# Optimization experiments

Hardware: AMD Instinct MI355X
Metric: run time of the kernel (lower is better)

The kernel has to match this reference:

```python
import jax, jax.numpy as jnp
import numpy as np

HIDDEN = 2048
N_HEADS = 16
N_KV = 4
HEAD_DIM = 128
SEQ = 2048
BATCH = 2
THETA = 10000.0


def rotate_half(x):
    half = x.shape[-1] // 2
    x1, x2 = x[..., :half], x[..., half:]
    return jnp.concatenate((-x2, x1), axis=-1)


def rope_cos_sin(seq_len, dim, theta, dtype):
    inv_freq = 1.0 / (theta ** (jnp.arange(0, dim, 2, dtype=jnp.float32) / dim))
    t = jnp.arange(seq_len, dtype=jnp.float32)
    freqs = jnp.einsum('i,j->ij', t, inv_freq)            # [S, dim/2]
    emb = jnp.concatenate((freqs, freqs), axis=-1)        # [S, dim]
    return jnp.cos(emb).astype(dtype), jnp.sin(emb).astype(dtype)


def setup_inputs() -> dict:
    key = jax.random.key(0)
    kx, kq, kk, kv, ko = jax.random.split(key, 5)
    s = 0.02
    return {
        'x':  jax.random.normal(kx, (BATCH, SEQ, HIDDEN), dtype=jnp.float32),
        'Wq': jax.random.normal(kq, (HIDDEN, N_HEADS * HEAD_DIM), dtype=jnp.float32) * s,
        'Wk': jax.random.normal(kk, (HIDDEN, N_KV * HEAD_DIM), dtype=jnp.float32) * s,
        'Wv': jax.random.normal(kv, (HIDDEN, N_KV * HEAD_DIM), dtype=jnp.float32) * s,
        'Wo': jax.random.normal(ko, (N_HEADS * HEAD_DIM, HIDDEN), dtype=jnp.float32) * s,
    }


def reference(x, Wq, Wk, Wv, Wo):
    B, S, _ = x.shape
    q = (x @ Wq).reshape(B, S, N_HEADS, HEAD_DIM)
    k = (x @ Wk).reshape(B, S, N_KV, HEAD_DIM)
    v = (x @ Wv).reshape(B, S, N_KV, HEAD_DIM)

    cos, sin = rope_cos_sin(S, HEAD_DIM, THETA, x.dtype)
    cos = cos[None, :, None, :]  # [1,S,1,D]
    sin = sin[None, :, None, :]
    q = q * cos + rotate_half(q) * sin
    k = k * cos + rotate_half(k) * sin

    repeat = N_HEADS // N_KV
    k = jnp.repeat(k, repeat, axis=2)  # repeat_interleave over heads
    v = jnp.repeat(v, repeat, axis=2)

    # [B,H,S,D]
    q = q.transpose(0, 2, 1, 3)
    k = k.transpose(0, 2, 1, 3)
    v = v.transpose(0, 2, 1, 3)

    scale = HEAD_DIM ** -0.5
    scores = jnp.einsum('bhqd,bhkd->bhqk', q, k) * scale
    causal = jnp.triu(jnp.full((S, S), -jnp.inf, dtype=scores.dtype), k=1)
    scores = scores + causal
    probs = jax.nn.softmax(scores, axis=-1)
    out = jnp.einsum('bhqk,bhkd->bhqd', probs, v)
    out = out.transpose(0, 2, 1, 3).reshape(B, S, N_HEADS * HEAD_DIM)
    return out @ Wo
```

## Files before the change

### kernel.cpp

```cpp
#include <hip/hip_runtime.h>
#include <hip/hip_bf16.h>
#include <math.h>

#define HIDDEN 2048
#define NHEADS 16
#define NKV 4
#define HD 128
#define SEQ 2048
#define BATCH 2
#define MTOT (BATCH*SEQ)
#define NQ (NHEADS*HD)
#define NKVD (NKV*HD)
#define NQKV (NQ + 2*NKVD)

typedef __attribute__((ext_vector_type(8))) short short8;
typedef __attribute__((ext_vector_type(4))) float float4v;

#if __has_builtin(__builtin_amdgcn_exp2f)
#define EXP2F __builtin_amdgcn_exp2f
#else
#define EXP2F exp2f
#endif
#define C1 0.1275174f

static __device__ __forceinline__ unsigned short f2bf(float f) {
  union { float f; unsigned int u; } v; v.f = f;
  unsigned int r = v.u + 0x7FFF + ((v.u >> 16) & 1);
  return (unsigned short)(r >> 16);
}
static __device__ __forceinline__ float bf2f(unsigned short h) {
  union { unsigned int u; float f; } v; v.u = ((unsigned int)h) << 16;
  return v.f;
}

static __device__ __forceinline__ void async16(const unsigned short* g, unsigned short* l) {
  __builtin_amdgcn_global_load_lds(
      (const __attribute__((address_space(1))) unsigned int*)g,
      (__attribute__((address_space(3))) unsigned int*)l, 16, 0, 0);
}

__global__ void cast_f32_bf16(const float* __restrict__ in,
                              unsigned short* __restrict__ out, int n) {
  int i = (blockIdx.x * blockDim.x + threadIdx.x) * 4;
  if (i < n) {
    float4 v = *(const float4*)(in + i);
    ushort4 o;
    o.x = f2bf(v.x); o.y = f2bf(v.y); o.z = f2bf(v.z); o.w = f2bf(v.w);
    *(ushort4*)(out + i) = o;
  }
}

__global__ void transpose_cast_all(
    const float* __restrict__ Wq, const float* __restrict__ Wk,
    const float* __restrict__ Wv, const float* __restrict__ Wo,
    unsigned short* __restrict__ Wqt, unsigned short* __restrict__ Wkt,
    unsigned short* __restrict__ Wvt, unsigned short* __restrict__ Wot) {
  __shared__ float tile[32][33];
  const int K = 2048;
  int bx = blockIdx.x;
  const float* W; unsigned short* Wt; int N; int tn;
  if (bx < 64)      { W = Wq; Wt = Wqt; N = NQ;     tn = bx * 32; }
  else if (bx < 80) { W = Wk; Wt = Wkt; N = NKVD;   tn = (bx - 64) * 32; }
  else if (bx < 96) { W = Wv; Wt = Wvt; N = NKVD;   tn = (bx - 80) * 32; }
  else              { W = Wo; Wt = Wot; N = HIDDEN; tn = (bx - 96) * 32; }
  int tk = blockIdx.y * 32;
  int tx = threadIdx.x & 31;
  int ty = threadIdx.x >> 5;
  #pragma unroll
  for (int i = 0; i < 4; i++) {
    int k = tk + ty + i * 8;
    tile[ty + i * 8][tx] = W[(size_t)k * N + tn + tx];
  }
  __syncthreads();
  #pragma unroll
  for (int i = 0; i < 4; i++) {
    int n = tn + ty + i * 8;
    Wt[(size_t)n * K + tk + tx] = f2bf(tile[tx][ty + i * 8]);
  }
}

__global__ void rope_all(unsigned short* __restrict__ Qb,
                         unsigned short* __restrict__ Kb) {
  int idx = blockIdx.x * blockDim.x + threadIdx.x;
  const int QTOT = MTOT * NHEADS * 64;
  unsigned short* P; int nheads;
  if (idx < QTOT) { P = Qb; nheads = NHEADS; }
  else            { P = Kb; nheads = NKV; idx -= QTOT; }
  int d = idx & 63;
  int hr = idx >> 6;
  int spos = (hr / nheads) % SEQ;
  size_t base = (size_t)hr * HD;
  float inv = exp2f((float)d * -0.2076205059304601f);
  float ang = (float)spos * inv;
  float sn, cs;
  sincosf(ang, &sn, &cs);
  float q1 = bf2f(P[base + d]);
  float q2 = bf2f(P[base + d + 64]);
  P[base + d]      = f2bf(q1 * cs - q2 * sn);
  P[base + d + 64] = f2bf(q2 * cs + q1 * sn);
}

__global__ __launch_bounds__(512, 2) void gemm_qkv(
    const unsigned short* __restrict__ A,
    const unsigned short* __restrict__ Bt,
    unsigned short* __restrict__ Qb,
    unsigned short* __restrict__ Kb,
    unsigned short* __restrict__ Vt) {
  __shared__ __align__(16) unsigned short L[4 * 16384];
  const int K = HIDDEN;
  const int NT = K / 32;
  int bm = blockIdx.y * 256, bn = blockIdx.x * 256;
  int tid = threadIdx.x, w = tid >> 6, lane = tid & 63;
  int wrow = w >> 2, wcol = w & 3;
  int m16 = lane & 15, quad = lane >> 4;
  int lrow = lane >> 2, lch = lane & 3;
  int lchs = lch ^ ((lrow >> 1) & 3);
  int qx = quad ^ ((m16 >> 1) & 3);
  const unsigned short* Ag = A + (size_t)(bm + w * 32 + lrow) * K + lchs * 8;
  const unsigned short* Bg = Bt + (size_t)(bn + w * 32 + lrow) * K + lchs * 8;

  float4v acc[8][4];
  #pragma unroll
  for (int i = 0; i < 8; i++)
    #pragma unroll
    for (int j = 0; j < 4; j++) acc[i][j] = (float4v)0.0f;

  auto stage = [&](int t) {
    unsigned short* Lb = L + (t & 3) * 16384;
    int k0 = t * 32;
    #pragma unroll
    for (int i = 0; i < 2; i++) {
      async16(Ag + (size_t)i * 16 * K + k0, Lb + w * 1024 + i * 512);
      async16(Bg + (size_t)i * 16 * K + k0, Lb + 8192 + w * 1024 + i * 512);
    }
  };

  const bool isV = (blockIdx.x >= 10);

  stage(0); stage(1);
  asm volatile("s_waitcnt vmcnt(4)" ::: "memory");
  __builtin_amdgcn_s_barrier();
  __builtin_amdgcn_sched_barrier(0);

  if (!isV) {
    for (int t = 0; t < NT; ++t) {
      if (t + 2 < NT) stage(t + 2);
      const unsigned short* Ab_ = L + (t & 3) * 16384;
      const unsigned short* Bb_ = Ab_ + 8192;
      short8 af[8], bfr[4];
      #pragma unroll
      for (int i = 0; i < 8; i++)
        af[i] = *(const short8*)(&Ab_[(wrow * 128 + i * 16 + m16) * 32 + qx * 8]);
      #pragma unroll
      for (int j = 0; j < 4; j++)
        bfr[j] = *(const short8*)(&Bb_[(wcol * 64 + j * 16 + m16) * 32 + qx * 8]);
      __builtin_amdgcn_s_setprio(1);
      #pragma unroll
      for (int i = 0; i < 8; i++)
        #pragma unroll
        for (int j = 0; j < 4; j++)
          acc[i][j] = __builtin_amdgcn_mfma_f32_16x16x32_bf16(af[i], bfr[j], acc[i][j], 0, 0, 0);
      __builtin_amdgcn_s_setprio(0);
      if (t + 2 < NT) { asm volatile("s_waitcnt vmcnt(4)" ::: "memory"); }
      else            { asm volatile("s_waitcnt vmcnt(0)" ::: "memory"); }
      __builtin_amdgcn_s_barrier();
      __builtin_amdgcn_sched_barrier(0);
    }
  } else {
    for (int t = 0; t < NT; ++t) {
      if (t + 2 < NT) stage(t + 2);
      const unsigned short* Ab_ = L + (t & 3) * 16384;
      const unsigned short* Bb_ = Ab_ + 8192;
      short8 af[8], bfr[4];
      #pragma unroll
      for (int i = 0; i < 8; i++)
        af[i] = *(const short8*)(&Ab_[(wrow * 128 + i * 16 + m16) * 32 + qx * 8]);
      #pragma unroll
      for (int j = 0; j < 4; j++)
        bfr[j] = *(const short8*)(&Bb_[(wcol * 64 + j * 16 + m16) * 32 + qx * 8]);
      __builtin_amdgcn_s_setprio(1);
      #pragma unroll
      for (int i = 0; i < 8; i++)
        #pragma unroll
        for (int j = 0; j < 4; j++)
          acc[i][j] = __builtin_amdgcn_mfma_f32_16x16x32_bf16(bfr[j], af[i], acc[i][j], 0, 0, 0);
      __builtin_amdgcn_s_setprio(0);
      if (t + 2 < NT) { asm volatile("s_waitcnt vmcnt(4)" ::: "memory"); }
      else            { asm volatile("s_waitcnt vmcnt(0)" ::: "memory"); }
      __builtin_amdgcn_s_barrier();
      __builtin_amdgcn_sched_barrier(0);
    }
  }

  if (blockIdx.x < 8) {
    #pragma unroll
    for (int i = 0; i < 8; i++)
      #pragma unroll
      for (int j = 0; j < 4; j++)
        #pragma unroll
        for (int r = 0; r < 4; r++) {
          int row = bm + wrow * 128 + i * 16 + quad * 4 + r;
          int col = bn + wcol * 64 + j * 16 + m16;
          Qb[(size_t)row * NQ + col] = f2bf(acc[i][j][r]);
        }
  } else if (!isV) {
    #pragma unroll
    for (int i = 0; i < 8; i++)
      #pragma unroll
      for (int j = 0; j < 4; j++)
        #pragma unroll
        for (int r = 0; r < 4; r++) {
          int row = bm + wrow * 128 + i * 16 + quad * 4 + r;
          int col = bn - 2048 + wcol * 64 + j * 16 + m16;
          Kb[(size_t)row * NKVD + col] = f2bf(acc[i][j][r]);
        }
  } else {
    #pragma unroll
    for (int i = 0; i < 8; i++)
      #pragma unroll
      for (int j = 0; j < 4; j++)
        #pragma unroll
        for (int r = 0; r < 4; r++) {
          int f = bn - 2560 + wcol * 64 + j * 16 + quad * 4 + r;
          int m = bm + wrow * 128 + i * 16 + m16;
          Vt[(size_t)f * MTOT + m] = f2bf(acc[i][j][r]);
        }
  }
}

__global__ __launch_bounds__(256, 2) void gemm_o(
    const unsigned short* __restrict__ A,
    const unsigned short* __restrict__ Bt,
    float* __restrict__ C, int M, int N, int K) {
  __shared__ __align__(16) unsigned short L[4 * 8192];
  const int NT = K / 32;
  int bm = blockIdx.y * 128, bn = blockIdx.x * 128;
  int tid = threadIdx.x, w = tid >> 6, lane = tid & 63;
  int wm = (w >> 1) * 64, wn = (w & 1) * 64;
  int m16 = lane & 15, quad = lane >> 4;
  int lrow = lane >> 2, lch = lane & 3;
  int lchs = lch ^ ((lrow >> 1) & 3);
  int qx = quad ^ ((m16 >> 1) & 3);
  const unsigned short* Ag = A + (size_t)(bm + w * 32 + lrow) * K + lchs * 8;
  const unsigned short* Bg = Bt + (size_t)(bn + w * 32 + lrow) * K + lchs * 8;

  float4v acc[4][4];
  #pragma unroll
  for (int i = 0; i < 4; i++)
    #pragma unroll
    for (int j = 0; j < 4; j++) acc[i][j] = (float4v)0.0f;

  auto stage = [&](int t) {
    unsigned short* Lb = L + (t & 3) * 8192;
    int k0 = t * 32;
    #pragma unroll
    for (int i = 0; i < 2; i++) {
      async16(Ag + (size_t)i * 16 * K + k0, Lb + w * 1024 + i * 512);
      async16(Bg + (size_t)i * 16 * K + k0, Lb + 4096 + w * 1024 + i * 512);
    }
  };

  stage(0); stage(1);
  asm volatile("s_waitcnt vmcnt(4)" ::: "memory");
  __builtin_amdgcn_s_barrier();
  __builtin_amdgcn_sched_barrier(0);

  for (int t = 0; t < NT; ++t) {
    if (t + 2 < NT) stage(t + 2);
    const unsigned short* Ab_ = L + (t & 3) * 8192;
    const unsigned short* Bb_ = Ab_ + 4096;
    short8 af[4], bfr[4];
    #pragma unroll
    for (int i = 0; i < 4; i++)
      af[i] = *(const short8*)(&Ab_[(wm + i * 16 + m16) * 32 + qx * 8]);
    #pragma unroll
    for (int j = 0; j < 4; j++)
      bfr[j] = *(const short8*)(&Bb_[(wn + j * 16 + m16) * 32 + qx * 8]);
    __builtin_amdgcn_s_setprio(1);
    #pragma unroll
    for (int i = 0; i < 4; i++)
      #pragma unroll
      for (int j = 0; j < 4; j++)
        acc[i][j] = __builtin_amdgcn_mfma_f32_16x16x32_bf16(af[i], bfr[j], acc[i][j], 0, 0, 0);
    __builtin_amdgcn_s_setprio(0);
    if (t + 2 < NT) { asm volatile("s_waitcnt vmcnt(4)" ::: "memory"); }
    else            { asm volatile("s_waitcnt vmcnt(0)" ::: "memory"); }
    __builtin_amdgcn_s_barrier();
    __builtin_amdgcn_sched_barrier(0);
  }

  #pragma unroll
  for (int i = 0; i < 4; i++)
    #pragma unroll
    for (int j = 0; j < 4; j++)
      #pragma unroll
      for (int r = 0; r < 4; r++) {
        int row = bm + wm + i * 16 + quad * 4 + r;
        int col = bn + wn + j * 16 + m16;
        C[(size_t)row * N + col] = acc[i][j][r];
      }
}

#define FLASH_TILE(CUR, NXT)                                                  \
  {                                                                           \
    const int ktb = kt * 64;                                                  \
    __syncthreads();        \
    {                                                                         \
      const unsigned short* Vg = Vt + vgrow * (size_t)MTOT                    \
                                    + (size_t)b * SEQ + ktb + kcv * 32 + vlch * 8; \
      unsigned short* Vl = Vs + kcv * 4096 + ipv * 512;                       \
      _Pragma("unroll")                                                       \
      for (int i = 0; i < 4; i++) async16(Vg + (size_t)i * 16 * MTOT, Vl + i * 512); \
    }                                                                         \
    if (kt < H) {                                                             \
      const unsigned short* Kg = Kp + (((size_t)b * SEQ + (kt + 1) * 64 + lrow) * NKV + kvh) * HD + w * 32 + vlch * 8; \
      unsigned short* Kl = NXT + w * 2048;                                    \
      _Pragma("unroll")                                                       \
      for (int i = 0; i < 4; i++) async16(Kg + (size_t)i * 16 * NKV * HD, Kl + i * 512); \
    }                                                                         \
    const bool act1 = (ktb <= lmax_w);                                        \
    float4v sacc[2][4];                                                       \
    _Pragma("unroll") for (int s4 = 0; s4 < 4; s4++) {                        \
      sacc[0][s4] = (float4v)0.0f; sacc[1][s4] = (float4v)0.0f; }             \
    __builtin_amdgcn_s_setprio(1);                                            \
    if (act1) {                                                               \
      _Pragma("unroll")                                                       \
      for (int s4 = 0; s4 < 4; s4++)                                          \
        _Pragma("unroll")                                                     \
        for (int c = 0; c < 4; c++) {                                         \
          short8 kf = *(const short8*)(&CUR[c * 2048 + (s4 * 16 + m16) * 32 + qx * 8]); \
          sacc[0][s4] = __builtin_amdgcn_mfma_f32_16x16x32_bf16(kf, qf[0][c], sacc[0][s4], 0, 0, 0); \
          sacc[1][s4] = __builtin_amdgcn_mfma_f32_16x16x32_bf16(kf, qf[1][c], sacc[1][s4], 0, 0, 0); \
        }                                                                     \
    } else {                                                                  \
      _Pragma("unroll")                                                       \
      for (int s4 = 0; s4 < 4; s4++)                                          \
        _Pragma("unroll")                                                     \
        for (int c = 0; c < 4; c++) {                                         \
          short8 kf = *(const short8*)(&CUR[c * 2048 + (s4 * 16 + m16) * 32 + qx * 8]); \
          sacc[0][s4] = __builtin_amdgcn_mfma_f32_16x16x32_bf16(kf, qf[0][c], sacc[0][s4], 0, 0, 0); \
        }                                                                     \
    }                                                                         \
    __builtin_amdgcn_s_setprio(0);                                            \
    _Pragma("unroll")                                                         \
    for (int qs = 0; qs < 2; qs++) {                                          \
      if (qs == 0 || act1) {                                                  \
        const int tb = qs ? L : H;                                            \
        const int qabs = tb * 64 + w * 16 + m16;                              \
        const bool diag = (kt == tb);                                         \
        float sv[4][4]; float mloc = -1e30f;                                  \
        if (diag) {                                                           \
          _Pragma("unroll") for (int s4 = 0; s4 < 4; s4++)                    \
            _Pragma("unroll") for (int r = 0; r < 4; r++) {                   \
              int kabs = ktb + s4 * 16 + quad * 4 + r;                        \
              float t = sacc[qs][s4][r];                                      \
              sv[s4][r] = (kabs > qabs) ? -1e30f : t;                         \
              mloc = fmaxf(mloc, sv[s4][r]); }                                \
        } else {                                                              \
          _Pragma("unroll") for (int s4 = 0; s4 < 4; s4++)                    \
            _Pragma("unroll") for (int r = 0; r < 4; r++) {                   \
              sv[s4][r] = sacc[qs][s4][r]; mloc = fmaxf(mloc, sv[s4][r]); }   \
        }                                                                     \
        mloc *= C1;                                                           \
        mloc = fmaxf(mloc, __shfl_xor(mloc, 16, 64));                         \
        mloc = fmaxf(mloc, __shfl_xor(mloc, 32, 64));                         \
        float mnewS = fmaxf(miS[qs], mloc);                                   \
        const bool defer = (bool)__all(mloc <= miS[qs] + 8.0f);               \
        if (defer) mnewS = miS[qs];  \
        const int prow = qs * 64 + w * 16 + m16;                              \
        const int psw = prow * 32; const int rx = prow & 7;                   \
        float rs = 0.0f;                                                      \
        _Pragma("unroll") for (int s4 = 0; s4 < 4; s4++) {                    \
          float p0 = EXP2F(__builtin_fmaf(sv[s4][0], C1, -mnewS));            \
          float p1 = EXP2F(__builtin_fmaf(sv[s4][1], C1, -mnewS));            \
          float p2 = EXP2F(__builtin_fmaf(sv[s4][2], C1, -mnewS));            \
          float p3 = EXP2F(__builtin_fmaf(sv[s4][3], C1, -mnewS));            \
          rs += p0 + p1 + p2 + p3;                                            \
          uint2 u;                                                            \
          u.x = (__float_as_uint(p1) & 0xffff0000u) | (__float_as_uint(p0) >> 16); \
          u.y = (__float_as_uint(p3) & 0xffff0000u) | (__float_as_uint(p2) >> 16); \
          int chunkW = s4 * 2 + (quad >> 1);                                  \
          *(uint2*)(&Ps[psw + ((chunkW ^ rx) << 2) + (quad & 1) * 2]) = u;    \
        }                                                                     \
        rs += __shfl_xor(rs, 16, 64);                                         \
        rs += __shfl_xor(rs, 32, 64);                                         \
        if (!defer) {                                                         \
          const float alpha = EXP2F(miS[qs] - mnewS);                         \
          li[qs] *= alpha; miS[qs] = mnewS;                                   \
          _Pragma("unroll") for (int ds = 0; ds < 8; ds++) oacc[ds][qs] *= alpha; \
        }                                                                     \
        li[qs] += rs;                                                         \
      }                                                                       \
    }                                                                         \
    __syncthreads();     \
    {                                                                         \
      const int r0 = w * 16 + m16, r1 = 64 + w * 16 + m16;                    \
      __builtin_amdgcn_s_setprio(1);                                          \
      if (act1) {                                                             \
        _Pragma("unroll")                                                     \
        for (int kc = 0; kc < 2; kc++) {                                      \
          short8 pf0 = *(const short8*)(&Ps[r0 * 32 + (((kc * 4 + quad) ^ (r0 & 7)) << 2)]); \
          short8 pf1 = *(const short8*)(&Ps[r1 * 32 + (((kc * 4 + quad) ^ (r1 & 7)) << 2)]); \
          _Pragma("unroll")                                                   \
          for (int ds = 0; ds < 8; ds++) {                                    \
            short8 vf = *(const short8*)(&Vs[kc * 4096 + (ds * 16 + m16) * 32 + qx * 8]); \
            oacc[ds][0] = __builtin_amdgcn_mfma_f32_16x16x32_bf16(vf, pf0, oacc[ds][0], 0, 0, 0); \
            oacc[ds][1] = __builtin_amdgcn_mfma_f32_16x16x32_bf16(vf, pf1, oacc[ds][1], 0, 0, 0); \
          }                                                                   \
        }                                                                     \
      } else {                                                                \
        _Pragma("unroll")                                                     \
        for (int kc = 0; kc < 2; kc++) {                                      \
          short8 pf0 = *(const short8*)(&Ps[r0 * 32 + (((kc * 4 + quad) ^ (r0 & 7)) << 2)]); \
          _Pragma("unroll")                                                   \
          for (int ds = 0; ds < 8; ds++) {                                    \
            short8 vf = *(const short8*)(&Vs[kc * 4096 + (ds * 16 + m16) * 32 + qx * 8]); \
            oacc[ds][0] = __builtin_amdgcn_mfma_f32_16x16x32_bf16(vf, pf0, oacc[ds][0], 0, 0, 0); \
          }                                                                   \
        }                                                                     \
      }                                                                       \
      __builtin_amdgcn_s_setprio(0);                                          \
    }                                                                         \
  }

__global__ __launch_bounds__(256, 2) void flash_attn(
    const unsigned short* __restrict__ Q,
    const unsigned short* __restrict__ Kp,
    const unsigned short* __restrict__ Vt,
    unsigned short* __restrict__ O) {
  __shared__ unsigned short Ks0[4 * 64 * 32];
  __shared__ unsigned short Ks1[4 * 64 * 32];
  __shared__ unsigned short Vs[2 * 128 * 32];
  __shared__ unsigned int   Ps[128 * 32];

  int bx = blockIdx.x;
  int h  = blockIdx.y;
  int b  = blockIdx.z;
  int kvh = h >> 2;
  int H = 31 - bx, L = bx;
  int tid = threadIdx.x;
  int w = tid >> 6, lane = tid & 63;
  int m16 = lane & 15, quad = lane >> 4;
  int lrow = lane >> 2, lch = lane & 3;
  const int vlch = lch ^ ((lrow >> 1) & 3);
  const int qx = quad ^ ((m16 >> 1) & 3);
  const int lmax_w = L * 64 + w * 16 + 15;

  const int kcv = w >> 1, ipv = (w & 1) * 4;
  const size_t vgrow = (size_t)kvh * HD + ipv * 16 + lrow;

  short8 qf[2][4];
  #pragma unroll
  for (int qs = 0; qs < 2; qs++) {
    int tb = qs ? L : H;
    size_t qbase = (((size_t)b * SEQ + tb * 64 + w * 16 + m16) * NHEADS + h) * HD;
    #pragma unroll
    for (int c = 0; c < 4; c++)
      qf[qs][c] = *(const short8*)(Q + qbase + c * 32 + quad * 8);
  }

  float4v oacc[8][2];
  #pragma unroll
  for (int ds = 0; ds < 8; ds++) { oacc[ds][0] = (float4v)0.0f; oacc[ds][1] = (float4v)0.0f; }
  float miS[2] = {-1e30f, -1e30f}, li[2] = {0.0f, 0.0f};

  {
    const unsigned short* Kg = Kp + (((size_t)b * SEQ + lrow) * NKV + kvh) * HD + w * 32 + vlch * 8;
    unsigned short* Kl = Ks0 + w * 2048;
    #pragma unroll
    for (int i = 0; i < 4; i++) async16(Kg + (size_t)i * 16 * NKV * HD, Kl + i * 512);
  }

  int kt = 0;
  for (;;) {
    FLASH_TILE(Ks0, Ks1)
    if (++kt > H) break;
    FLASH_TILE(Ks1, Ks0)
    if (++kt > H) break;
  }

  #pragma unroll
  for (int qs = 0; qs < 2; qs++) {
    float inv = 1.0f / li[qs];
    int tb = qs ? L : H;
    int qabs = tb * 64 + w * 16 + m16;
    size_t obase = (((size_t)b * SEQ + qabs) * NHEADS + h) * HD + quad * 4;
    #pragma unroll
    for (int ds = 0; ds < 8; ds++) {
      float v0 = oacc[ds][qs][0] * inv;
      float v1 = oacc[ds][qs][1] * inv;
      float v2 = oacc[ds][qs][2] * inv;
      float v3 = oacc[ds][qs][3] * inv;
      uint2 u;
      u.x = ((unsigned)f2bf(v1) << 16) | f2bf(v0);
      u.y = ((unsigned)f2bf(v3) << 16) | f2bf(v2);
      *(uint2*)(O + obase + ds * 16) = u;
    }
  }
}

extern "C" void kernel_launch(void* const* d_in, const int* in_sizes, int n_in,
                              void* d_out, int out_size, void* d_ws, size_t ws_size,
                              hipStream_t stream) {
  const float* x  = (const float*)d_in[0];
  const float* Wq = (const float*)d_in[1];
  const float* Wk = (const float*)d_in[2];
  const float* Wv = (const float*)d_in[3];
  const float* Wo = (const float*)d_in[4];
  float* out = (float*)d_out;

  unsigned short* ws = (unsigned short*)d_ws;
  unsigned short* xb  = ws;
  unsigned short* Wqt = xb  + (size_t)MTOT * HIDDEN;
  unsigned short* Wkt = Wqt + (size_t)NQ * HIDDEN;
  unsigned short* Wvt = Wkt + (size_t)NKVD * HIDDEN;
  unsigned short* Wot = Wvt + (size_t)NKVD * HIDDEN;
  unsigned short* Qb  = Wot + (size_t)NQ * HIDDEN;
  unsigned short* Kb  = Qb  + (size_t)MTOT * NQ;
  unsigned short* Vtb = Kb  + (size_t)MTOT * NKVD;
  unsigned short* Ab  = Vtb + (size_t)MTOT * NKVD;

  cast_f32_bf16<<<(MTOT * HIDDEN / 4 + 255) / 256, 256, 0, stream>>>(x, xb, MTOT * HIDDEN);
  transpose_cast_all<<<dim3(160, 64), 256, 0, stream>>>(Wq, Wk, Wv, Wo, Wqt, Wkt, Wvt, Wot);

  gemm_qkv<<<dim3(NQKV / 256, MTOT / 256), 512, 0, stream>>>(xb, Wqt, Qb, Kb, Vtb);

  rope_all<<<(MTOT * (NHEADS + NKV) * 64) / 256, 256, 0, stream>>>(Qb, Kb);

  flash_attn<<<dim3(16, NHEADS, BATCH), 256, 0, stream>>>(Qb, Kb, Vtb, Ab);

  gemm_o<<<dim3(HIDDEN / 128, MTOT / 128), 256, 0, stream>>>(Ab, Wot, out, MTOT, HIDDEN, NQ);
}
```

Measured before the change: 286.3 us.

## Merge prep kernels, fuse Q RoPE into attention, double GEMM wave counts

Merges the x cast and weight transpose-cast into one prep launch. Q RoPE is now applied in registers inside flash attention, so rope only runs on K, which removes a full read and write pass over Q. Both GEMMs double threads per block (1024 and 512) and give each wave a smaller sub-tile, with one async load per thread per stage. This trades fewer launches and less Q traffic for per-wave sincos work in attention and different GEMM occupancy and register behaviour.

```diff
diff --git a/kernel.cpp b/kernel.cpp
--- a/kernel.cpp
+++ b/kernel.cpp
@@ -39,31 +39,30 @@
       (__attribute__((address_space(3))) unsigned int*)l, 16, 0, 0);
 }
 
-__global__ void cast_f32_bf16(const float* __restrict__ in,
-                              unsigned short* __restrict__ out, int n) {
-  int i = (blockIdx.x * blockDim.x + threadIdx.x) * 4;
-  if (i < n) {
-    float4 v = *(const float4*)(in + i);
+__global__ void prep(const float* __restrict__ x, unsigned short* __restrict__ xb,
+                     const float* __restrict__ Wq, const float* __restrict__ Wk,
+                     const float* __restrict__ Wv, const float* __restrict__ Wo,
+                     unsigned short* __restrict__ Wqt, unsigned short* __restrict__ Wkt,
+                     unsigned short* __restrict__ Wvt, unsigned short* __restrict__ Wot) {
+  __shared__ float tile[32][33];
+  int bx = blockIdx.x;
+  if (bx < 8192) {
+    int i = (bx * 256 + threadIdx.x) * 4;
+    float4 v = *(const float4*)(x + i);
     ushort4 o;
     o.x = f2bf(v.x); o.y = f2bf(v.y); o.z = f2bf(v.z); o.w = f2bf(v.w);
-    *(ushort4*)(out + i) = o;
-  }
-}
-
-__global__ void transpose_cast_all(
-    const float* __restrict__ Wq, const float* __restrict__ Wk,
-    const float* __restrict__ Wv, const float* __restrict__ Wo,
-    unsigned short* __restrict__ Wqt, unsigned short* __restrict__ Wkt,
-    unsigned short* __restrict__ Wvt, unsigned short* __restrict__ Wot) {
-  __shared__ float tile[32][33];
+    *(ushort4*)(xb + i) = o;
+    return;
+  }
+  int bz = bx - 8192;
+  int tbx = bz % 160, tby = bz / 160;
   const int K = 2048;
-  int bx = blockIdx.x;
   const float* W; unsigned short* Wt; int N; int tn;
-  if (bx < 64)      { W = Wq; Wt = Wqt; N = NQ;     tn = bx * 32; }
-  else if (bx < 80) { W = Wk; Wt = Wkt; N = NKVD;   tn = (bx - 64) * 32; }
-  else if (bx < 96) { W = Wv; Wt = Wvt; N = NKVD;   tn = (bx - 80) * 32; }
-  else              { W = Wo; Wt = Wot; N = HIDDEN; tn = (bx - 96) * 32; }
-  int tk = blockIdx.y * 32;
+  if (tbx < 64)      { W = Wq; Wt = Wqt; N = NQ;     tn = tbx * 32; }
+  else if (tbx < 80) { W = Wk; Wt = Wkt; N = NKVD;   tn = (tbx - 64) * 32; }
+  else if (tbx < 96) { W = Wv; Wt = Wvt; N = NKVD;   tn = (tbx - 80) * 32; }
+  else               { W = Wo; Wt = Wot; N = HIDDEN; tn = (tbx - 96) * 32; }
+  int tk = tby * 32;
   int tx = threadIdx.x & 31;
   int ty = threadIdx.x >> 5;
   #pragma unroll
@@ -79,28 +78,23 @@
   }
 }
 
-__global__ void rope_all(unsigned short* __restrict__ Qb,
-                         unsigned short* __restrict__ Kb) {
+__global__ void rope_k(unsigned short* __restrict__ Kb) {
   int idx = blockIdx.x * blockDim.x + threadIdx.x;
-  const int QTOT = MTOT * NHEADS * 64;
-  unsigned short* P; int nheads;
-  if (idx < QTOT) { P = Qb; nheads = NHEADS; }
-  else            { P = Kb; nheads = NKV; idx -= QTOT; }
   int d = idx & 63;
   int hr = idx >> 6;
-  int spos = (hr / nheads) % SEQ;
+  int spos = (hr / NKV) % SEQ;
   size_t base = (size_t)hr * HD;
   float inv = exp2f((float)d * -0.2076205059304601f);
   float ang = (float)spos * inv;
   float sn, cs;
   sincosf(ang, &sn, &cs);
-  float q1 = bf2f(P[base + d]);
-  float q2 = bf2f(P[base + d + 64]);
-  P[base + d]      = f2bf(q1 * cs - q2 * sn);
-  P[base + d + 64] = f2bf(q2 * cs + q1 * sn);
-}
-
-__global__ __launch_bounds__(512, 2) void gemm_qkv(
+  float q1 = bf2f(Kb[base + d]);
+  float q2 = bf2f(Kb[base + d + 64]);
+  Kb[base + d]      = f2bf(q1 * cs - q2 * sn);
+  Kb[base + d + 64] = f2bf(q2 * cs + q1 * sn);
+}
+
+__global__ __launch_bounds__(1024, 4) void gemm_qkv(
     const unsigned short* __restrict__ A,
     const unsigned short* __restrict__ Bt,
     unsigned short* __restrict__ Qb,
@@ -113,32 +107,29 @@
   int tid = threadIdx.x, w = tid >> 6, lane = tid & 63;
   int wrow = w >> 2, wcol = w & 3;
   int m16 = lane & 15, quad = lane >> 4;
-  int lrow = lane >> 2, lch = lane & 3;
-  int lchs = lch ^ ((lrow >> 1) & 3);
+  int r = tid >> 2, lch = tid & 3;
+  int lchs = lch ^ ((r >> 1) & 3);
   int qx = quad ^ ((m16 >> 1) & 3);
-  const unsigned short* Ag = A + (size_t)(bm + w * 32 + lrow) * K + lchs * 8;
-  const unsigned short* Bg = Bt + (size_t)(bn + w * 32 + lrow) * K + lchs * 8;
-
-  float4v acc[8][4];
-  #pragma unroll
-  for (int i = 0; i < 8; i++)
+  const unsigned short* Agp = A + (size_t)(bm + r) * K + lchs * 8;
+  const unsigned short* Bgp = Bt + (size_t)(bn + r) * K + lchs * 8;
+
+  float4v acc[4][4];
+  #pragma unroll
+  for (int i = 0; i < 4; i++)
     #pragma unroll
     for (int j = 0; j < 4; j++) acc[i][j] = (float4v)0.0f;
 
   auto stage = [&](int t) {
     unsigned short* Lb = L + (t & 3) * 16384;
     int k0 = t * 32;
-    #pragma unroll
-    for (int i = 0; i < 2; i++) {
-      async16(Ag + (size_t)i * 16 * K + k0, Lb + w * 1024 + i * 512);
-      async16(Bg + (size_t)i * 16 * K + k0, Lb + 8192 + w * 1024 + i * 512);
-    }
+    async16(Agp + k0, Lb + tid * 8);
+    async16(Bgp + k0, Lb + 8192 + tid * 8);
   };
 
   const bool isV = (blockIdx.x >= 10);
 
   stage(0); stage(1);
-  asm volatile("s_waitcnt vmcnt(4)" ::: "memory");
+  asm volatile("s_waitcnt vmcnt(2)" ::: "memory");
   __builtin_amdgcn_s_barrier();
   __builtin_amdgcn_sched_barrier(0);
 
@@ -147,21 +138,21 @@
       if (t + 2 < NT) stage(t + 2);
       const unsigned short* Ab_ = L + (t & 3) * 16384;
       const unsigned short* Bb_ = Ab_ + 8192;
-      short8 af[8], bfr[4];
-      #pragma unroll
-      for (int i = 0; i < 8; i++)
-        af[i] = *(const short8*)(&Ab_[(wrow * 128 + i * 16 + m16) * 32 + qx * 8]);
+      short8 af[4], bfr[4];
+      #pragma unroll
+      for (int i = 0; i < 4; i++)
+        af[i] = *(const short8*)(&Ab_[(wrow * 64 + i * 16 + m16) * 32 + qx * 8]);
       #pragma unroll
       for (int j = 0; j < 4; j++)
         bfr[j] = *(const short8*)(&Bb_[(wcol * 64 + j * 16 + m16) * 32 + qx * 8]);
       __builtin_amdgcn_s_setprio(1);
       #pragma unroll
-      for (int i = 0; i < 8; i++)
+      for (int i = 0; i < 4; i++)
         #pragma unroll
         for (int j = 0; j < 4; j++)
           acc[i][j] = __builtin_amdgcn_mfma_f32_16x16x32_bf16(af[i], bfr[j], acc[i][j], 0, 0, 0);
       __builtin_amdgcn_s_setprio(0);
-      if (t + 2 < NT) { asm volatile("s_waitcnt vmcnt(4)" ::: "memory"); }
+      if (t + 2 < NT) { asm volatile("s_waitcnt vmcnt(2)" ::: "memory"); }
       else            { asm volatile("s_waitcnt vmcnt(0)" ::: "memory"); }
       __builtin_amdgcn_s_barrier();
       __builtin_amdgcn_sched_barrier(0);
@@ -171,21 +162,21 @@
       if (t + 2 < NT) stage(t + 2);
       const unsigned short* Ab_ = L + (t & 3) * 16384;
       const unsigned short* Bb_ = Ab_ + 8192;
-      short8 af[8], bfr[4];
-      #pragma unroll
-      for (int i = 0; i < 8; i++)
-        af[i] = *(const short8*)(&Ab_[(wrow * 128 + i * 16 + m16) * 32 + qx * 8]);
+      short8 af[4], bfr[4];
+      #pragma unroll
+      for (int i = 0; i < 4; i++)
+        af[i] = *(const short8*)(&Ab_[(wrow * 64 + i * 16 + m16) * 32 + qx * 8]);
       #pragma unroll
       for (int j = 0; j < 4; j++)
         bfr[j] = *(const short8*)(&Bb_[(wcol * 64 + j * 16 + m16) * 32 + qx * 8]);
       __builtin_amdgcn_s_setprio(1);
       #pragma unroll
-      for (int i = 0; i < 8; i++)
+      for (int i = 0; i < 4; i++)
         #pragma unroll
         for (int j = 0; j < 4; j++)
           acc[i][j] = __builtin_amdgcn_mfma_f32_16x16x32_bf16(bfr[j], af[i], acc[i][j], 0, 0, 0);
       __builtin_amdgcn_s_setprio(0);
-      if (t + 2 < NT) { asm volatile("s_waitcnt vmcnt(4)" ::: "memory"); }
+      if (t + 2 < NT) { asm volatile("s_waitcnt vmcnt(2)" ::: "memory"); }
       else            { asm volatile("s_waitcnt vmcnt(0)" ::: "memory"); }
       __builtin_amdgcn_s_barrier();
       __builtin_amdgcn_sched_barrier(0);
@@ -194,41 +185,41 @@
 
   if (blockIdx.x < 8) {
     #pragma unroll
-    for (int i = 0; i < 8; i++)
+    for (int i = 0; i < 4; i++)
       #pragma unroll
       for (int j = 0; j < 4; j++)
         #pragma unroll
-        for (int r = 0; r < 4; r++) {
-          int row = bm + wrow * 128 + i * 16 + quad * 4 + r;
+        for (int rr = 0; rr < 4; rr++) {
+          int row = bm + wrow * 64 + i * 16 + quad * 4 + rr;
           int col = bn + wcol * 64 + j * 16 + m16;
-          Qb[(size_t)row * NQ + col] = f2bf(acc[i][j][r]);
+          Qb[(size_t)row * NQ + col] = f2bf(acc[i][j][rr]);
         }
   } else if (!isV) {
     #pragma unroll
-    for (int i = 0; i < 8; i++)
+    for (int i = 0; i < 4; i++)
       #pragma unroll
       for (int j = 0; j < 4; j++)
         #pragma unroll
-        for (int r = 0; r < 4; r++) {
-          int row = bm + wrow * 128 + i * 16 + quad * 4 + r;
+        for (int rr = 0; rr < 4; rr++) {
+          int row = bm + wrow * 64 + i * 16 + quad * 4 + rr;
           int col = bn - 2048 + wcol * 64 + j * 16 + m16;
-          Kb[(size_t)row * NKVD + col] = f2bf(acc[i][j][r]);
+          Kb[(size_t)row * NKVD + col] = f2bf(acc[i][j][rr]);
         }
   } else {
     #pragma unroll
-    for (int i = 0; i < 8; i++)
+    for (int i = 0; i < 4; i++)
       #pragma unroll
       for (int j = 0; j < 4; j++)
         #pragma unroll
-        for (int r = 0; r < 4; r++) {
-          int f = bn - 2560 + wcol * 64 + j * 16 + quad * 4 + r;
-          int m = bm + wrow * 128 + i * 16 + m16;
-          Vt[(size_t)f * MTOT + m] = f2bf(acc[i][j][r]);
+        for (int rr = 0; rr < 4; rr++) {
+          int f = bn - 2560 + wcol * 64 + j * 16 + quad * 4 + rr;
+          int m = bm + wrow * 64 + i * 16 + m16;
+          Vt[(size_t)f * MTOT + m] = f2bf(acc[i][j][rr]);
         }
   }
 }
 
-__global__ __launch_bounds__(256, 2) void gemm_o(
+__global__ __launch_bounds__(512, 4) void gemm_o(
     const unsigned short* __restrict__ A,
     const unsigned short* __restrict__ Bt,
     float* __restrict__ C, int M, int N, int K) {
@@ -236,32 +227,29 @@
   const int NT = K / 32;
   int bm = blockIdx.y * 128, bn = blockIdx.x * 128;
   int tid = threadIdx.x, w = tid >> 6, lane = tid & 63;
-  int wm = (w >> 1) * 64, wn = (w & 1) * 64;
+  int wrow = w >> 2, wcol = w & 3;
   int m16 = lane & 15, quad = lane >> 4;
-  int lrow = lane >> 2, lch = lane & 3;
-  int lchs = lch ^ ((lrow >> 1) & 3);
+  int r = tid >> 2, lch = tid & 3;
+  int lchs = lch ^ ((r >> 1) & 3);
   int qx = quad ^ ((m16 >> 1) & 3);
-  const unsigned short* Ag = A + (size_t)(bm + w * 32 + lrow) * K + lchs * 8;
-  const unsigned short* Bg = Bt + (size_t)(bn + w * 32 + lrow) * K + lchs * 8;
-
-  float4v acc[4][4];
+  const unsigned short* Agp = A + (size_t)(bm + r) * K + lchs * 8;
+  const unsigned short* Bgp = Bt + (size_t)(bn + r) * K + lchs * 8;
+
+  float4v acc[4][2];
   #pragma unroll
   for (int i = 0; i < 4; i++)
     #pragma unroll
-    for (int j = 0; j < 4; j++) acc[i][j] = (float4v)0.0f;
+    for (int j = 0; j < 2; j++) acc[i][j] = (float4v)0.0f;
 
   auto stage = [&](int t) {
     unsigned short* Lb = L + (t & 3) * 8192;
     int k0 = t * 32;
-    #pragma unroll
-    for (int i = 0; i < 2; i++) {
-      async16(Ag + (size_t)i * 16 * K + k0, Lb + w * 1024 + i * 512);
-      async16(Bg + (size_t)i * 16 * K + k0, Lb + 4096 + w * 1024 + i * 512);
-    }
+    async16(Agp + k0, Lb + tid * 8);
+    async16(Bgp + k0, Lb + 4096 + tid * 8);
   };
 
   stage(0); stage(1);
-  asm volatile("s_waitcnt vmcnt(4)" ::: "memory");
+  asm volatile("s_waitcnt vmcnt(2)" ::: "memory");
   __builtin_amdgcn_s_barrier();
   __builtin_amdgcn_sched_barrier(0);
 
@@ -269,21 +257,21 @@
     if (t + 2 < NT) stage(t + 2);
     const unsigned short* Ab_ = L + (t & 3) * 8192;
     const unsigned short* Bb_ = Ab_ + 4096;
-    short8 af[4], bfr[4];
+    short8 af[4], bfr[2];
     #pragma unroll
     for (int i = 0; i < 4; i++)
-      af[i] = *(const short8*)(&Ab_[(wm + i * 16 + m16) * 32 + qx * 8]);
-    #pragma unroll
-    for (int j = 0; j < 4; j++)
-      bfr[j] = *(const short8*)(&Bb_[(wn + j * 16 + m16) * 32 + qx * 8]);
+      af[i] = *(const short8*)(&Ab_[(wrow * 64 + i * 16 + m16) * 32 + qx * 8]);
+    #pragma unroll
+    for (int j = 0; j < 2; j++)
+      bfr[j] = *(const short8*)(&Bb_[(wcol * 32 + j * 16 + m16) * 32 + qx * 8]);
     __builtin_amdgcn_s_setprio(1);
     #pragma unroll
     for (int i = 0; i < 4; i++)
       #pragma unroll
-      for (int j = 0; j < 4; j++)
+      for (int j = 0; j < 2; j++)
         acc[i][j] = __builtin_amdgcn_mfma_f32_16x16x32_bf16(af[i], bfr[j], acc[i][j], 0, 0, 0);
     __builtin_amdgcn_s_setprio(0);
-    if (t + 2 < NT) { asm volatile("s_waitcnt vmcnt(4)" ::: "memory"); }
+    if (t + 2 < NT) { asm volatile("s_waitcnt vmcnt(2)" ::: "memory"); }
     else            { asm volatile("s_waitcnt vmcnt(0)" ::: "memory"); }
     __builtin_amdgcn_s_barrier();
     __builtin_amdgcn_sched_barrier(0);
@@ -292,12 +280,12 @@
   #pragma unroll
   for (int i = 0; i < 4; i++)
     #pragma unroll
-    for (int j = 0; j < 4; j++)
-      #pragma unroll
-      for (int r = 0; r < 4; r++) {
-        int row = bm + wm + i * 16 + quad * 4 + r;
-        int col = bn + wn + j * 16 + m16;
-        C[(size_t)row * N + col] = acc[i][j][r];
+    for (int j = 0; j < 2; j++)
+      #pragma unroll
+      for (int rr = 0; rr < 4; rr++) {
+        int row = bm + wrow * 64 + i * 16 + quad * 4 + rr;
+        int col = bn + wcol * 32 + j * 16 + m16;
+        C[(size_t)row * N + col] = acc[i][j][rr];
       }
 }
 
@@ -351,15 +339,15 @@
         float sv[4][4]; float mloc = -1e30f;                                  \
         if (diag) {                                                           \
           _Pragma("unroll") for (int s4 = 0; s4 < 4; s4++)                    \
-            _Pragma("unroll") for (int r = 0; r < 4; r++) {                   \
-              int kabs = ktb + s4 * 16 + quad * 4 + r;                        \
-              float t = sacc[qs][s4][r];                                      \
-              sv[s4][r] = (kabs > qabs) ? -1e30f : t;                         \
-              mloc = fmaxf(mloc, sv[s4][r]); }                                \
+            _Pragma("unroll") for (int rr = 0; rr < 4; rr++) {                \
+              int kabs = ktb + s4 * 16 + quad * 4 + rr;                       \
+              float t = sacc[qs][s4][rr];                                     \
+              sv[s4][rr] = (kabs > qabs) ? -1e30f : t;                        \
+              mloc = fmaxf(mloc, sv[s4][rr]); }                               \
         } else {                                                              \
           _Pragma("unroll") for (int s4 = 0; s4 < 4; s4++)                    \
-            _Pragma("unroll") for (int r = 0; r < 4; r++) {                   \
-              sv[s4][r] = sacc[qs][s4][r]; mloc = fmaxf(mloc, sv[s4][r]); }   \
+            _Pragma("unroll") for (int rr = 0; rr < 4; rr++) {                \
+              sv[s4][rr] = sacc[qs][s4][rr]; mloc = fmaxf(mloc, sv[s4][rr]); } \
         }                                                                     \
         mloc *= C1;                                                           \
         mloc = fmaxf(mloc, __shfl_xor(mloc, 16, 64));                         \
@@ -458,6 +446,26 @@
     for (int c = 0; c < 4; c++)
       qf[qs][c] = *(const short8*)(Q + qbase + c * 32 + quad * 8);
   }
+  #pragma unroll
+  for (int qs = 0; qs < 2; qs++) {
+    int tb = qs ? L : H;
+    float spos = (float)(tb * 64 + w * 16 + m16);
+    #pragma unroll
+    for (int c = 0; c < 2; c++) {
+      #pragma unroll
+      for (int e = 0; e < 8; e++) {
+        int d = c * 32 + quad * 8 + e;
+        float inv = exp2f((float)d * -0.2076205059304601f);
+        float ang = spos * inv;
+        float sn, cs;
+        sincosf(ang, &sn, &cs);
+        float f1 = bf2f((unsigned short)qf[qs][c][e]);
+        float f2 = bf2f((unsigned short)qf[qs][c + 2][e]);
+        qf[qs][c][e]     = (short)f2bf(f1 * cs - f2 * sn);
+        qf[qs][c + 2][e] = (short)f2bf(f2 * cs + f1 * sn);
+      }
+    }
+  }
 
   float4v oacc[8][2];
   #pragma unroll
@@ -520,14 +528,13 @@
   unsigned short* Vtb = Kb  + (size_t)MTOT * NKVD;
   unsigned short* Ab  = Vtb + (size_t)MTOT * NKVD;
 
-  cast_f32_bf16<<<(MTOT * HIDDEN / 4 + 255) / 256, 256, 0, stream>>>(x, xb, MTOT * HIDDEN);
-  transpose_cast_all<<<dim3(160, 64), 256, 0, stream>>>(Wq, Wk, Wv, Wo, Wqt, Wkt, Wvt, Wot);
-
-  gemm_qkv<<<dim3(NQKV / 256, MTOT / 256), 512, 0, stream>>>(xb, Wqt, Qb, Kb, Vtb);
-
-  rope_all<<<(MTOT * (NHEADS + NKV) * 64) / 256, 256, 0, stream>>>(Qb, Kb);
+  prep<<<8192 + 160 * 64, 256, 0, stream>>>(x, xb, Wq, Wk, Wv, Wo, Wqt, Wkt, Wvt, Wot);
+
+  gemm_qkv<<<dim3(NQKV / 256, MTOT / 256), 1024, 0, stream>>>(xb, Wqt, Qb, Kb, Vtb);
+
+  rope_k<<<(MTOT * NKV * 64) / 256, 256, 0, stream>>>(Kb);
 
   flash_attn<<<dim3(16, NHEADS, BATCH), 256, 0, stream>>>(Qb, Kb, Vtb, Ab);
 
-  gemm_o<<<dim3(HIDDEN / 128, MTOT / 128), 256, 0, stream>>>(Ab, Wot, out, MTOT, HIDDEN, NQ);
-}
+  gemm_o<<<dim3(HIDDEN / 128, MTOT / 128), 512, 0, stream>>>(Ab, Wot, out, MTOT, HIDDEN, NQ);
+}
```

New measurement: 276.1 us. -3.6%, faster.
